# Kernel optimization log

Hardware: AMD Instinct MI355X
Metric: run time of the kernel (lower is better)

## Reference

```python
import jax, jax.numpy as jnp
import numpy as np

N = 50000      # nodes
E = 800000     # edges (avg degree 16)
IN = 128       # in_channels
C = 64         # hidden_channels (per-head out channels)
H = 8          # heads


def _lin(key, fan_in, fan_out):
    kw, kb = jax.random.split(key)
    scale = 1.0 / np.sqrt(fan_in)
    W = jax.random.uniform(kw, (fan_in, fan_out), jnp.float32, -scale, scale)
    b = jax.random.uniform(kb, (fan_out,), jnp.float32, -scale, scale)
    return W, b


def setup_inputs() -> dict:
    key = jax.random.key(0)
    ks = jax.random.split(key, 16)
    inp = {
        'x': jax.random.normal(ks[0], (N, IN), jnp.float32),
        'edge_index': jax.random.randint(ks[1], (2, E), 0, N, jnp.int64),
    }
    # layer 0: IN -> H*C (concat), layer 1: H*C -> H*C (concat), layer 2: H*C -> C (heads=1)
    dims = [(IN, H * C, H * C), (H * C, H * C, H * C), (H * C, C, C)]
    k = 2
    for i, (fi, fqkv, fskip) in enumerate(dims):
        for nm, fo in (('Wq', fqkv), ('Wk', fqkv), ('Wv', fqkv), ('Ws', fskip)):
            W, b = _lin(ks[k], fi, fo)
            inp[f'{nm}{i}'] = W
            inp[f'b{nm[1]}{i}'] = b
            k += 1
    return inp


def _conv(x, src, dst, Wq, bq, Wk, bk, Wv, bv, Ws, bs, heads, ch, concat):
    n = x.shape[0]
    q = (x @ Wq + bq).reshape(n, heads, ch)   # [N,H,C]
    k = (x @ Wk + bk).reshape(n, heads, ch)
    v = (x @ Wv + bv).reshape(n, heads, ch)
    # per-edge attention logits: [E,H]
    alpha = jnp.einsum('ehc,ehc->eh', q[dst], k[src]) / (ch ** 0.5)
    # segment softmax over incoming edges of each target node
    m = jax.ops.segment_max(alpha, dst, num_segments=n)
    m = jnp.where(jnp.isfinite(m), m, 0.0)
    ea = jnp.exp(alpha - m[dst])
    denom = jax.ops.segment_sum(ea, dst, num_segments=n) + 1e-16
    attn = ea / denom[dst]                    # [E,H]
    out = jax.ops.segment_sum(attn[:, :, None] * v[src], dst, num_segments=n)  # [N,H,C]
    out = out.reshape(n, heads * ch) if concat else out.mean(axis=1)
    # root/skip connection (beta=False)
    return out + x @ Ws + bs


def reference(x, edge_index,
              Wq0, bq0, Wk0, bk0, Wv0, bv0, Ws0, bs0,
              Wq1, bq1, Wk1, bk1, Wv1, bv1, Ws1, bs1,
              Wq2, bq2, Wk2, bk2, Wv2, bv2, Ws2, bs2):
    src, dst = edge_index[0], edge_index[1]
    h = _conv(x, src, dst, Wq0, bq0, Wk0, bk0, Wv0, bv0, Ws0, bs0, H, C, True)
    h = jax.nn.relu(h)
    h = _conv(h, src, dst, Wq1, bq1, Wk1, bk1, Wv1, bv1, Ws1, bs1, H, C, True)
    h = jax.nn.relu(h)
    out = _conv(h, src, dst, Wq2, bq2, Wk2, bk2, Wv2, bv2, Ws2, bs2, 1, C, False)
    return out
```

## Files before the change

### kernel.cpp

```cpp
#include <hip/hip_runtime.h>
#include <hip/hip_fp16.h>
#include <math.h>
#include <stdio.h>


using f16x8 = __attribute__((ext_vector_type(8))) _Float16;
using f32x4 = __attribute__((ext_vector_type(4))) float;

__device__ __forceinline__ void load_lds16(const void* g, void* l) {
  __builtin_amdgcn_global_load_lds((const __attribute__((address_space(1))) void*)g,
                                   (__attribute__((address_space(3))) void*)l,
                                   16, 0, 0);
}

__device__ __forceinline__ void fp8x4_to_f32(unsigned int w, float* o4) {
#if __has_builtin(__builtin_amdgcn_cvt_pk_f32_fp8)
  auto lo = __builtin_amdgcn_cvt_pk_f32_fp8(w, false);
  auto hi = __builtin_amdgcn_cvt_pk_f32_fp8(w, true);
  o4[0] = lo[0]; o4[1] = lo[1]; o4[2] = hi[0]; o4[3] = hi[1];
#else
#pragma unroll
  for (int t = 0; t < 4; ++t) {
    unsigned int b = (w >> (8 * t)) & 0xFFu;
    unsigned short h = (unsigned short)(((b & 0x80u) << 8) | ((b & 0x7Fu) << 7));
    __half hv = *(__half*)&h;
    o4[t] = (float)hv * 256.0f;
  }
#endif
}

__device__ __forceinline__ unsigned int fp8_pack2_sw(float a, float b) {
  unsigned int r = 0;
#pragma unroll
  for (int t = 0; t < 2; ++t) {
    float f = t ? b : a;
    __half h = __float2half(f * (1.0f / 256.0f));
    unsigned short hb = *(unsigned short*)&h;
    unsigned int sign = (hb >> 8) & 0x80u;
    unsigned int mag = (hb & 0x7FFFu) + 0x40u;
    unsigned int e = (mag >> 7) & 0x7Fu;
    if ((mag >> 7) > 0x7Eu) e = 0x7Eu;
    r |= (sign | e) << (8 * t);
  }
  return r;
}

__device__ __forceinline__ uint2 fp8_pack8(const float* f) {
#if __has_builtin(__builtin_amdgcn_cvt_pk_fp8_f32)
  int w0 = __builtin_amdgcn_cvt_pk_fp8_f32(f[0], f[1], 0, false);
  w0 = __builtin_amdgcn_cvt_pk_fp8_f32(f[2], f[3], w0, true);
  int w1 = __builtin_amdgcn_cvt_pk_fp8_f32(f[4], f[5], 0, false);
  w1 = __builtin_amdgcn_cvt_pk_fp8_f32(f[6], f[7], w1, true);
  uint2 r; r.x = (unsigned)w0; r.y = (unsigned)w1; return r;
#else
  uint2 r;
  r.x = fp8_pack2_sw(f[0], f[1]) | (fp8_pack2_sw(f[2], f[3]) << 16);
  r.y = fp8_pack2_sw(f[4], f[5]) | (fp8_pack2_sw(f[6], f[7]) << 16);
  return r;
#endif
}

__global__ void zero_misc_kernel(int* __restrict__ deg, __half* __restrict__ H,
                                 int N, int Npad) {
  int t = blockIdx.x * 256 + threadIdx.x;
  if (t < N) deg[t] = 0;
  int nz = (Npad - N) * 512 / 8;
  if (t < nz) {
    f16x8 z = {};
    *(f16x8*)(H + (size_t)N * 512 + (size_t)t * 8) = z;
  }
}

__global__ void degree_kernel(const int* __restrict__ dst, int* __restrict__ deg, int E) {
  int e = blockIdx.x * blockDim.x + threadIdx.x;
  if (e < E) atomicAdd(&deg[dst[e]], 1);
}

__global__ __launch_bounds__(256)
void scan_a_kernel(const int* __restrict__ deg, int* __restrict__ rowptr,
                   int* __restrict__ bsum, int n) {
  __shared__ int tmp[256];
  int t = threadIdx.x;
  int i = blockIdx.x * 256 + t;
  int v = (i < n) ? deg[i] : 0;
  tmp[t] = v;
  __syncthreads();
#pragma unroll
  for (int off = 1; off < 256; off <<= 1) {
    int u = (t >= off) ? tmp[t - off] : 0;
    __syncthreads();
    tmp[t] += u;
    __syncthreads();
  }
  if (i < n) rowptr[i + 1] = tmp[t];
  if (t == 255) bsum[blockIdx.x] = tmp[255];
}

__global__ __launch_bounds__(256)
void scan_b_kernel(int* __restrict__ bsum, int nb) {
  __shared__ int tmp[256];
  int t = threadIdx.x;
  int v = (t < nb) ? bsum[t] : 0;
  tmp[t] = v;
  __syncthreads();
#pragma unroll
  for (int off = 1; off < 256; off <<= 1) {
    int u = (t >= off) ? tmp[t - off] : 0;
    __syncthreads();
    tmp[t] += u;
    __syncthreads();
  }
  if (t < nb) bsum[t] = tmp[t] - v;
}

__global__ __launch_bounds__(256)
void scan_c_kernel(int* __restrict__ rowptr, int* __restrict__ cursor,
                   const int* __restrict__ bsum, int n) {
  int i = blockIdx.x * 256 + threadIdx.x;
  if (i < n) {
    int r = rowptr[i + 1] + bsum[blockIdx.x];
    rowptr[i + 1] = r;
    cursor[i + 1] = r;
  }
  if (i == 0) { rowptr[0] = 0; cursor[0] = 0; }
}

__global__ void scatter_kernel(const int* __restrict__ src, const int* __restrict__ dst,
                               int* __restrict__ cursor, int* __restrict__ col, int E) {
  int e = blockIdx.x * blockDim.x + threadIdx.x;
  if (e < E) {
    int pos = atomicAdd(&cursor[dst[e]], 1);
    col[pos] = src[e];
  }
}

__global__ __launch_bounds__(256)
void transpose_all_kernel(
    const float* __restrict__ Wq0, const float* __restrict__ Wk0,
    const float* __restrict__ Wv0, const float* __restrict__ Ws0,
    const float* __restrict__ Wq1, const float* __restrict__ Wk1,
    const float* __restrict__ Wv1, const float* __restrict__ Ws1,
    const float* __restrict__ Wq2, const float* __restrict__ Wk2,
    const float* __restrict__ Wv2, const float* __restrict__ Ws2,
    __half* __restrict__ Wt) {
  int z = blockIdx.z;
  int layer = z >> 2, m = z & 3;
  int K = (layer == 0) ? 128 : 512;
  int D = (layer == 2) ? 64 : 512;
  int c0 = blockIdx.x * 32, k0 = blockIdx.y * 32;
  if (c0 >= D || k0 >= K) return;
  const float* W;
  switch (z) {
    case 0: W = Wq0; break; case 1: W = Wk0; break;
    case 2: W = Wv0; break; case 3: W = Ws0; break;
    case 4: W = Wq1; break; case 5: W = Wk1; break;
    case 6: W = Wv1; break; case 7: W = Ws1; break;
    case 8: W = Wq2; break; case 9: W = Wk2; break;
    case 10: W = Wv2; break; default: W = Ws2; break;
  }
  __half* dstBase = Wt + ((layer == 0) ? 0 : (layer == 1) ? 262144 : 1310720);
  __shared__ float t[32][33];
  int tx = threadIdx.x & 31, ty = threadIdx.x >> 5;
#pragma unroll
  for (int r = 0; r < 4; ++r)
    t[ty + 8 * r][tx] = W[(size_t)(k0 + ty + 8 * r) * D + c0 + tx];
  __syncthreads();
#pragma unroll
  for (int r = 0; r < 4; ++r)
    dstBase[(size_t)(m * D + c0 + ty + 8 * r) * K + k0 + tx] =
        __float2half(t[tx][ty + 8 * r]);
}

__global__ void bias_all_kernel(
    const float* __restrict__ b0, const float* __restrict__ b1,
    const float* __restrict__ b2, const float* __restrict__ b3,
    const float* __restrict__ b4, const float* __restrict__ b5,
    const float* __restrict__ b6, const float* __restrict__ b7,
    const float* __restrict__ b8, const float* __restrict__ b9,
    const float* __restrict__ b10, const float* __restrict__ b11,
    float* __restrict__ bias_arena) {
  int z = blockIdx.x;
  int layer = z >> 2, m = z & 3;
  int D = (layer == 2) ? 64 : 512;
  const float* b;
  switch (z) {
    case 0: b = b0; break; case 1: b = b1; break;
    case 2: b = b2; break; case 3: b = b3; break;
    case 4: b = b4; break; case 5: b = b5; break;
    case 6: b = b6; break; case 7: b = b7; break;
    case 8: b = b8; break; case 9: b = b9; break;
    case 10: b = b10; break; default: b = b11; break;
  }
  float* dst = bias_arena + ((layer == 0) ? 0 : (layer == 1) ? 2048 : 4096) + m * D;
  for (int c = threadIdx.x; c < D; c += 256) dst[c] = b[c];
}

template <int LAYER>
__global__ __launch_bounds__(256, 2)
void gemm_mfma_kernel(const void* __restrict__ Avoid,
                      const __half* __restrict__ Wt,
                      const float* __restrict__ bias,
                      __half* __restrict__ QS, __half* __restrict__ KV,
                      int Nrows) {
  constexpr int K = (LAYER == 0) ? 128 : 512;
  constexpr int lda = (LAYER == 0) ? 128 : 512;
  constexpr int NT = (LAYER == 2) ? 1 : 8;
  constexpr int NSTEP = K / 32;
  __shared__ __align__(16) char smem_raw[49152];
  __half* sm = (__half*)smem_raw;
  int tid = threadIdx.x;
  int wave = tid >> 6, lane = tid & 63;
  int wr = wave >> 1, wc = wave & 1;
  int bid = blockIdx.x;
  int xcd = bid & 7;
  int r = bid >> 3;
  int n0 = (r % NT) * 256;
  int m0 = ((r / NT) * 8 + xcd) * 128;
  int srow = lane >> 2;
  int sslot = lane & 3;
  int skc = (sslot ^ ((srow >> 1) & 3)) << 3;
  int quad = lane >> 4, rr = lane & 15;
  int rslot = (quad ^ ((rr >> 1) & 3)) << 3;

  f32x4 acc[4][8] = {};

  auto stage = [&](int buf, int kt) {
    __half* As = sm + buf * 12288;
    __half* Bs = As + 4096;
#pragma unroll
    for (int p = 0; p < 2; ++p) {
      int rbase = wave * 32 + p * 16;
      if constexpr (LAYER == 0) {
        int row = m0 + rbase + srow;
        const float* ga = (const float*)Avoid + (size_t)row * lda + kt + skc;
        f16x8 hv = {};
        if (row < Nrows) {
          float4 f0 = *(const float4*)ga;
          float4 f1 = *(const float4*)(ga + 4);
          hv[0] = (_Float16)f0.x; hv[1] = (_Float16)f0.y;
          hv[2] = (_Float16)f0.z; hv[3] = (_Float16)f0.w;
          hv[4] = (_Float16)f1.x; hv[5] = (_Float16)f1.y;
          hv[6] = (_Float16)f1.z; hv[7] = (_Float16)f1.w;
        }
        *(f16x8*)&As[(rbase + srow) * 32 + sslot * 8] = hv;
      } else {
        const __half* ga = (const __half*)Avoid +
                           (size_t)(m0 + rbase + srow) * lda + kt + skc;
        load_lds16(ga, &As[rbase * 32]);
      }
    }
#pragma unroll
    for (int p = 0; p < 4; ++p) {
      int rbase = wave * 64 + p * 16;
      const __half* gb = Wt + (size_t)(n0 + rbase + srow) * K + kt + skc;
      load_lds16(gb, &Bs[rbase * 32]);
    }
  };

  stage(0, 0);
  __syncthreads();

  for (int t = 0; t < NSTEP; ++t) {
    if (t + 1 < NSTEP) stage((t + 1) & 1, (t + 1) * 32);
    const __half* As = sm + (t & 1) * 12288;
    const __half* Bs = As + 4096;
    f16x8 a[4], b[8];
#pragma unroll
    for (int i = 0; i < 4; ++i) {
      int row = wr * 64 + i * 16 + rr;
      a[i] = *(const f16x8*)&As[row * 32 + rslot];
    }
#pragma unroll
    for (int j = 0; j < 8; ++j) {
      int row = wc * 128 + j * 16 + rr;
      b[j] = *(const f16x8*)&Bs[row * 32 + rslot];
    }
#pragma unroll
    for (int i = 0; i < 4; ++i)
#pragma unroll
      for (int j = 0; j < 8; ++j)
        acc[i][j] = __builtin_amdgcn_mfma_f32_16x16x32_f16(a[i], b[j], acc[i][j], 0, 0, 0);
    __syncthreads();
  }

  int cl = lane & 15, rb = (lane >> 4) * 4;

  if constexpr (LAYER == 2) {
    __half* S = (__half*)smem_raw;
#pragma unroll
    for (int round = 0; round < 2; ++round) {
      if (wr == round) {
#pragma unroll
        for (int i = 0; i < 4; ++i)
#pragma unroll
          for (int j = 0; j < 8; ++j) {
            int colL = wc * 128 + j * 16 + cl;
            float bj = bias[colL];
#pragma unroll
            for (int rg = 0; rg < 4; ++rg) {
              int rowL = i * 16 + rb + rg;
              S[rowL * 264 + colL] = __float2half(acc[i][j][rg] + bj);
            }
          }
      }
      __syncthreads();
#pragma unroll
      for (int it = 0; it < 8; ++it) {
        int id = it * 256 + tid;
        int rowL = id >> 5, ch = id & 31;
        int grow = m0 + round * 64 + rowL;
        int colb = ch * 8;
        int seg = colb >> 6, c = colb & 63;
        __half* base = (seg == 0) ? QS + (size_t)grow * 128 + c
                     : (seg == 3) ? QS + (size_t)grow * 128 + 64 + c
                     : (seg == 1) ? KV + (size_t)grow * 128 + c
                                  : KV + (size_t)grow * 128 + 64 + c;
        *(f16x8*)base = *(const f16x8*)&S[rowL * 264 + colb];
      }
      __syncthreads();
    }
  } else {
    const int msegB = n0 >> 9;
    const int cb = n0 & 511;
    if (msegB == 0 || msegB == 3) {
      __half* S = (__half*)smem_raw;
      const int coff = (msegB == 3) ? 512 : 0;
#pragma unroll
      for (int round = 0; round < 2; ++round) {
        if (wr == round) {
#pragma unroll
          for (int i = 0; i < 4; ++i)
#pragma unroll
            for (int j = 0; j < 8; ++j) {
              int colL = wc * 128 + j * 16 + cl;
              float bj = bias[n0 + colL];
#pragma unroll
              for (int rg = 0; rg < 4; ++rg) {
                int rowL = i * 16 + rb + rg;
                S[rowL * 264 + colL] = __float2half(acc[i][j][rg] + bj);
              }
            }
        }
        __syncthreads();
#pragma unroll
        for (int it = 0; it < 8; ++it) {
          int id = it * 256 + tid;
          int rowL = id >> 5, ch = id & 31;
          int grow = m0 + round * 64 + rowL;
          int colb = ch * 8;
          *(f16x8*)(QS + (size_t)grow * 1024 + coff + cb + colb) =
              *(const f16x8*)&S[rowL * 264 + colb];
        }
        __syncthreads();
      }
    } else {
      float* S = (float*)smem_raw;
      unsigned char* KV8 = (unsigned char*)KV;
      const int koff = (msegB == 2) ? 8 : 0;
#pragma unroll
      for (int round = 0; round < 4; ++round) {
        if (wr == (round >> 1)) {
#pragma unroll
          for (int ii = 0; ii < 2; ++ii) {
#pragma unroll
            for (int j = 0; j < 8; ++j) {
              int colL = wc * 128 + j * 16 + cl;
              float bj = bias[n0 + colL];
#pragma unroll
              for (int rg = 0; rg < 4; ++rg) {
                int rowL = ii * 16 + rb + rg;
                S[rowL * 260 + colL] = acc[(round & 1) * 2 + ii][j][rg] + bj;
              }
            }
          }
        }
        __syncthreads();
#pragma unroll
        for (int it = 0; it < 4; ++it) {
          int id = it * 256 + tid;
          int rowL = id >> 5, ch = id & 31;
          int grow = m0 + round * 32 + rowL;
          int colb = ch * 8;
          float f[8];
          f32x4 lo = *(const f32x4*)&S[rowL * 260 + colb];
          f32x4 hi = *(const f32x4*)&S[rowL * 260 + colb + 4];
          f[0] = lo[0]; f[1] = lo[1]; f[2] = lo[2]; f[3] = lo[3];
          f[4] = hi[0]; f[5] = hi[1]; f[6] = hi[2]; f[7] = hi[3];
          uint2 pk = fp8_pack8(f);
          *(uint2*)(KV8 + (size_t)grow * 1024 + ((cb + colb) >> 3) * 16 + koff) = pk;
        }
        __syncthreads();
      }
    }
  }
}

__global__ __launch_bounds__(256)
void attn_h8_kernel(const __half* __restrict__ QS, const unsigned char* __restrict__ KV8,
                    const int* __restrict__ rowptr, const int* __restrict__ col,
                    __half* __restrict__ Hout, int N) {
  int n = blockIdx.x * 4 + (threadIdx.x >> 6);
  if (n >= N) return;
  int lane = threadIdx.x & 63;
  size_t rbase = (size_t)n * 1024 + lane * 8;

  f16x8 qv = __builtin_nontemporal_load((const f16x8*)(QS + rbase));
  float qf[8];
#pragma unroll
  for (int j = 0; j < 8; ++j) qf[j] = (float)qv[j];

  int e0 = rowptr[n], e1 = rowptr[n + 1];
  float m = -INFINITY, l = 0.f;
  float o[8] = {};

  const uint4* KVL = (const uint4*)KV8;
  uint4 ea = {}, eb = {};
  int i = e0;
  if (i < e1)     ea = KVL[(size_t)col[i] * 64 + lane];
  if (i + 1 < e1) eb = KVL[(size_t)col[i + 1] * 64 + lane];

  while (i < e1) {
    int rem = e1 - i;
    uint4 ec = {}, ed = {};
    if (rem > 2) ec = KVL[(size_t)col[i + 2] * 64 + lane];
    if (rem > 3) ed = KVL[(size_t)col[i + 3] * 64 + lane];
    float ka[8], kb[8];
    fp8x4_to_f32(ea.x, ka); fp8x4_to_f32(ea.y, ka + 4);
    fp8x4_to_f32(eb.x, kb); fp8x4_to_f32(eb.y, kb + 4);
    float pa = 0.f, pb = 0.f;
#pragma unroll
    for (int j = 0; j < 8; ++j) { pa += ka[j] * qf[j]; pb += kb[j] * qf[j]; }
    pa += __shfl_xor(pa, 1, 64); pb += __shfl_xor(pb, 1, 64);
    pa += __shfl_xor(pa, 2, 64); pb += __shfl_xor(pb, 2, 64);
    pa += __shfl_xor(pa, 4, 64); pb += __shfl_xor(pb, 4, 64);
    float a0 = pa * 0.125f;
    float va[8];
    fp8x4_to_f32(ea.z, va); fp8x4_to_f32(ea.w, va + 4);
    if (rem > 1) {
      float vb[8];
      fp8x4_to_f32(eb.z, vb); fp8x4_to_f32(eb.w, vb + 4);
      float a1 = pb * 0.125f;
      float mn = fmaxf(m, fmaxf(a0, a1));
      float sc = __expf(m - mn);
      float ex0 = __expf(a0 - mn), ex1 = __expf(a1 - mn);
      l = l * sc + ex0 + ex1;
#pragma unroll
      for (int c = 0; c < 8; ++c)
        o[c] = o[c] * sc + ex0 * va[c] + ex1 * vb[c];
      m = mn;
    } else {
      float mn = fmaxf(m, a0);
      float sc = __expf(m - mn);
      float ex0 = __expf(a0 - mn);
      l = l * sc + ex0;
#pragma unroll
      for (int c = 0; c < 8; ++c) o[c] = o[c] * sc + ex0 * va[c];
      m = mn;
    }
    ea = ec; eb = ed;
    i += 2;
  }

  float inv = 1.f / (l + 1e-16f);
  f16x8 sv = __builtin_nontemporal_load((const f16x8*)(QS + rbase + 512));
  f16x8 hv;
#pragma unroll
  for (int c = 0; c < 8; ++c) {
    float r = o[c] * inv + (float)sv[c];
    hv[c] = (_Float16)fmaxf(r, 0.f);
  }
  __builtin_nontemporal_store(hv, (f16x8*)(Hout + (size_t)n * 512 + lane * 8));
}

__global__ __launch_bounds__(256)
void attn_h1_kernel(const __half* __restrict__ QS, const __half* __restrict__ KV,
                    const int* __restrict__ rowptr, const int* __restrict__ col,
                    float* __restrict__ out, int N) {
  int n = (blockIdx.x * 256 + threadIdx.x) >> 3;
  if (n >= N) return;
  int gl = threadIdx.x & 7;
  size_t rbase = (size_t)n * 128 + gl * 8;

  f16x8 qv = __builtin_nontemporal_load((const f16x8*)(QS + rbase));
  float qf[8];
#pragma unroll
  for (int j = 0; j < 8; ++j) qf[j] = (float)qv[j];

  int e0 = rowptr[n], e1 = rowptr[n + 1];
  float m = -INFINITY, l = 0.f;
  float o[8] = {};

  f16x8 ka = {}, va = {}, kb = {}, vb = {};
  int i = e0;
  if (i < e1) {
    const __half* p = KV + (size_t)col[i] * 128 + gl * 8;
    ka = *(const f16x8*)p; va = *(const f16x8*)(p + 64);
  }
  if (i + 1 < e1) {
    const __half* p = KV + (size_t)col[i + 1] * 128 + gl * 8;
    kb = *(const f16x8*)p; vb = *(const f16x8*)(p + 64);
  }

  while (i < e1) {
    int rem = e1 - i;
    f16x8 kc = {}, vc = {}, kd = {}, vd = {};
    if (rem > 2) {
      const __half* p = KV + (size_t)col[i + 2] * 128 + gl * 8;
      kc = *(const f16x8*)p; vc = *(const f16x8*)(p + 64);
    }
    if (rem > 3) {
      const __half* p = KV + (size_t)col[i + 3] * 128 + gl * 8;
      kd = *(const f16x8*)p; vd = *(const f16x8*)(p + 64);
    }
    float pa = 0.f, pb = 0.f;
#pragma unroll
    for (int j = 0; j < 8; ++j) { pa += (float)ka[j] * qf[j]; pb += (float)kb[j] * qf[j]; }
    pa += __shfl_xor(pa, 1, 64); pb += __shfl_xor(pb, 1, 64);
    pa += __shfl_xor(pa, 2, 64); pb += __shfl_xor(pb, 2, 64);
    pa += __shfl_xor(pa, 4, 64); pb += __shfl_xor(pb, 4, 64);
    float a0 = pa * 0.125f;
    if (rem > 1) {
      float a1 = pb * 0.125f;
      float mn = fmaxf(m, fmaxf(a0, a1));
      float sc = __expf(m - mn);
      float ea = __expf(a0 - mn), eb = __expf(a1 - mn);
      l = l * sc + ea + eb;
#pragma unroll
      for (int c = 0; c < 8; ++c)
        o[c] = o[c] * sc + ea * (float)va[c] + eb * (float)vb[c];
      m = mn;
    } else {
      float mn = fmaxf(m, a0);
      float sc = __expf(m - mn);
      float ea = __expf(a0 - mn);
      l = l * sc + ea;
#pragma unroll
      for (int c = 0; c < 8; ++c) o[c] = o[c] * sc + ea * (float)va[c];
      m = mn;
    }
    ka = kc; va = vc; kb = kd; vb = vd;
    i += 2;
  }

  float inv = 1.f / (l + 1e-16f);
  f16x8 sv = __builtin_nontemporal_load((const f16x8*)(QS + rbase + 64));
  f32x4 r0, r1;
#pragma unroll
  for (int c = 0; c < 4; ++c) r0[c] = o[c] * inv + (float)sv[c];
#pragma unroll
  for (int c = 0; c < 4; ++c) r1[c] = o[c + 4] * inv + (float)sv[c + 4];
  float* op = out + (size_t)n * 64 + gl * 8;
  *(f32x4*)op = r0;
  *(f32x4*)(op + 4) = r1;
}

extern "C" void kernel_launch(void* const* d_in, const int* in_sizes, int n_in,
                              void* d_out, int out_size, void* d_ws, size_t ws_size,
                              hipStream_t stream) {
  const float* x = (const float*)d_in[0];
  const int* ei = (const int*)d_in[1];
  const int N = in_sizes[0] / 128;
  const int E = in_sizes[1] / 2;
  const int Npad = ((N + 1023) / 1024) * 1024;
  const int mtiles = Npad / 128;
  const int* srcp = ei;
  const int* dstp = ei + E;

  const float* Wq0 = (const float*)d_in[2];  const float* bq0 = (const float*)d_in[3];
  const float* Wk0 = (const float*)d_in[4];  const float* bk0 = (const float*)d_in[5];
  const float* Wv0 = (const float*)d_in[6];  const float* bv0 = (const float*)d_in[7];
  const float* Ws0 = (const float*)d_in[8];  const float* bs0 = (const float*)d_in[9];
  const float* Wq1 = (const float*)d_in[10]; const float* bq1 = (const float*)d_in[11];
  const float* Wk1 = (const float*)d_in[12]; const float* bk1 = (const float*)d_in[13];
  const float* Wv1 = (const float*)d_in[14]; const float* bv1 = (const float*)d_in[15];
  const float* Ws1 = (const float*)d_in[16]; const float* bs1 = (const float*)d_in[17];
  const float* Wq2 = (const float*)d_in[18]; const float* bq2 = (const float*)d_in[19];
  const float* Wk2 = (const float*)d_in[20]; const float* bk2 = (const float*)d_in[21];
  const float* Wv2 = (const float*)d_in[22]; const float* bv2 = (const float*)d_in[23];
  const float* Ws2 = (const float*)d_in[24]; const float* bs2 = (const float*)d_in[25];

  char* p = (char*)d_ws;
  __half* QS = (__half*)p;               p += (size_t)Npad * 1024 * 2;
  __half* KV = (__half*)p;               p += (size_t)Npad * 1024;
  __half* H  = (__half*)p;               p += (size_t)Npad * 512 * 2;
  __half* Wt = (__half*)p;               p += (size_t)1441792 * 2;
  float* bias_arena = (float*)p;         p += 4352 * 4;
  int* deg    = (int*)p;                 p += (size_t)N * 4;
  int* rowptr = (int*)p;                 p += (size_t)(N + 1) * 4;
  int* cursor = (int*)p;                 p += (size_t)(N + 1) * 4;
  int* colv   = (int*)p;                 p += (size_t)E * 4;
  int* bsum   = (int*)p;                 p += 256 * 4;
  size_t need = p - (char*)d_ws;
  if (ws_size < need) {
    fprintf(stderr, "kernel_launch: ws_size=%zu < need=%zu — aborting cleanly\n",
            ws_size, need);
    return;
  }

  const int nscan = (N + 255) / 256;

  transpose_all_kernel<<<dim3(16, 16, 12), 256, 0, stream>>>(
      Wq0, Wk0, Wv0, Ws0, Wq1, Wk1, Wv1, Ws1, Wq2, Wk2, Wv2, Ws2, Wt);
  bias_all_kernel<<<12, 256, 0, stream>>>(
      bq0, bk0, bv0, bs0, bq1, bk1, bv1, bs1, bq2, bk2, bv2, bs2, bias_arena);
  zero_misc_kernel<<<((Npad - N) * 512 / 8 + 255) / 256 > (N + 255) / 256
                         ? ((Npad - N) * 512 / 8 + 255) / 256
                         : (N + 255) / 256,
                    256, 0, stream>>>(deg, H, N, Npad);

  degree_kernel<<<(E + 255) / 256, 256, 0, stream>>>(dstp, deg, E);
  scan_a_kernel<<<nscan, 256, 0, stream>>>(deg, rowptr, bsum, N);
  scan_b_kernel<<<1, 256, 0, stream>>>(bsum, nscan);
  scan_c_kernel<<<nscan, 256, 0, stream>>>(rowptr, cursor, bsum, N);
  scatter_kernel<<<(E + 255) / 256, 256, 0, stream>>>(srcp, dstp, cursor, colv, E);

  __half* Wt0 = Wt;
  __half* Wt1 = Wt + 262144;
  __half* Wt2 = Wt + 1310720;

  gemm_mfma_kernel<0><<<mtiles * 8, 256, 0, stream>>>(
      x, Wt0, bias_arena, QS, KV, N);
  attn_h8_kernel<<<(N + 3) / 4, 256, 0, stream>>>(QS, (const unsigned char*)KV,
                                                  rowptr, colv, H, N);

  gemm_mfma_kernel<1><<<mtiles * 8, 256, 0, stream>>>(
      H, Wt1, bias_arena + 2048, QS, KV, Npad);
  attn_h8_kernel<<<(N + 3) / 4, 256, 0, stream>>>(QS, (const unsigned char*)KV,
                                                  rowptr, colv, H, N);

  gemm_mfma_kernel<2><<<mtiles, 256, 0, stream>>>(
      H, Wt2, bias_arena + 4096, QS, KV, Npad);
  attn_h1_kernel<<<(N + 31) / 32, 256, 0, stream>>>(QS, KV, rowptr, colv,
                                                    (float*)d_out, N);
}
```

Measured before the change: 747.1 us.

## Triple-buffer GEMM k-loop with async LDS loads and pre-convert x to fp16

The GEMM main loop moves from a double-buffered stage with full __syncthreads to a three-stage pipeline. It uses explicit vmcnt waits, split barriers and raised wave priority during the MFMA block, so global-to-LDS loads overlap more compute. Layer 0's input is converted to fp16 by a separate kernel, which lets all layers use the direct global_load_lds path. In exchange the LDS footprint grows to 72KB per block, which may cut occupancy below the launch bound of 2, and the extra conversion pass adds a launch and traffic.

```diff
diff --git a/kernel.cpp b/kernel.cpp
--- a/kernel.cpp
+++ b/kernel.cpp
@@ -69,6 +69,24 @@
     f16x8 z = {};
     *(f16x8*)(H + (size_t)N * 512 + (size_t)t * 8) = z;
   }
+}
+
+__global__ void convert_x_kernel(const float* __restrict__ x, __half* __restrict__ xh,
+                                 int N, int Npad) {
+  int t = blockIdx.x * 256 + threadIdx.x;
+  if (t >= Npad * 16) return;
+  int row = t >> 4;
+  f16x8 hv = {};
+  if (row < N) {
+    const float* g = x + (size_t)t * 8;
+    float4 f0 = *(const float4*)g;
+    float4 f1 = *(const float4*)(g + 4);
+    hv[0] = (_Float16)f0.x; hv[1] = (_Float16)f0.y;
+    hv[2] = (_Float16)f0.z; hv[3] = (_Float16)f0.w;
+    hv[4] = (_Float16)f1.x; hv[5] = (_Float16)f1.y;
+    hv[6] = (_Float16)f1.z; hv[7] = (_Float16)f1.w;
+  }
+  *(f16x8*)(xh + (size_t)t * 8) = hv;
 }
 
 __global__ void degree_kernel(const int* __restrict__ dst, int* __restrict__ deg, int E) {
@@ -197,16 +215,15 @@
 
 template <int LAYER>
 __global__ __launch_bounds__(256, 2)
-void gemm_mfma_kernel(const void* __restrict__ Avoid,
+void gemm_mfma_kernel(const __half* __restrict__ Aptr,
                       const __half* __restrict__ Wt,
                       const float* __restrict__ bias,
-                      __half* __restrict__ QS, __half* __restrict__ KV,
-                      int Nrows) {
+                      __half* __restrict__ QS, __half* __restrict__ KV) {
   constexpr int K = (LAYER == 0) ? 128 : 512;
   constexpr int lda = (LAYER == 0) ? 128 : 512;
   constexpr int NT = (LAYER == 2) ? 1 : 8;
   constexpr int NSTEP = K / 32;
-  __shared__ __align__(16) char smem_raw[49152];
+  __shared__ __align__(16) char smem_raw[73728];
   __half* sm = (__half*)smem_raw;
   int tid = threadIdx.x;
   int wave = tid >> 6, lane = tid & 63;
@@ -230,24 +247,8 @@
 #pragma unroll
     for (int p = 0; p < 2; ++p) {
       int rbase = wave * 32 + p * 16;
-      if constexpr (LAYER == 0) {
-        int row = m0 + rbase + srow;
-        const float* ga = (const float*)Avoid + (size_t)row * lda + kt + skc;
-        f16x8 hv = {};
-        if (row < Nrows) {
-          float4 f0 = *(const float4*)ga;
-          float4 f1 = *(const float4*)(ga + 4);
-          hv[0] = (_Float16)f0.x; hv[1] = (_Float16)f0.y;
-          hv[2] = (_Float16)f0.z; hv[3] = (_Float16)f0.w;
-          hv[4] = (_Float16)f1.x; hv[5] = (_Float16)f1.y;
-          hv[6] = (_Float16)f1.z; hv[7] = (_Float16)f1.w;
-        }
-        *(f16x8*)&As[(rbase + srow) * 32 + sslot * 8] = hv;
-      } else {
-        const __half* ga = (const __half*)Avoid +
-                           (size_t)(m0 + rbase + srow) * lda + kt + skc;
-        load_lds16(ga, &As[rbase * 32]);
-      }
+      const __half* ga = Aptr + (size_t)(m0 + rbase + srow) * lda + kt + skc;
+      load_lds16(ga, &As[rbase * 32]);
     }
 #pragma unroll
     for (int p = 0; p < 4; ++p) {
@@ -258,11 +259,16 @@
   };
 
   stage(0, 0);
-  __syncthreads();
+  stage(1, 32);
+  stage(2, 64);
 
   for (int t = 0; t < NSTEP; ++t) {
-    if (t + 1 < NSTEP) stage((t + 1) & 1, (t + 1) * 32);
-    const __half* As = sm + (t & 1) * 12288;
+    if (t + 2 < NSTEP)      asm volatile("s_waitcnt vmcnt(12)" ::: "memory");
+    else if (t + 1 < NSTEP) asm volatile("s_waitcnt vmcnt(6)" ::: "memory");
+    else                    asm volatile("s_waitcnt vmcnt(0)" ::: "memory");
+    __builtin_amdgcn_s_barrier();
+
+    const __half* As = sm + (t % 3) * 12288;
     const __half* Bs = As + 4096;
     f16x8 a[4], b[8];
 #pragma unroll
@@ -275,13 +281,21 @@
       int row = wc * 128 + j * 16 + rr;
       b[j] = *(const f16x8*)&Bs[row * 32 + rslot];
     }
+    asm volatile("s_waitcnt lgkmcnt(0)" ::: "memory");
+    __builtin_amdgcn_sched_barrier(0);
+    __builtin_amdgcn_s_barrier();
+
+    if (t + 3 < NSTEP) stage(t % 3, (t + 3) * 32);
+
+    __builtin_amdgcn_s_setprio(1);
 #pragma unroll
     for (int i = 0; i < 4; ++i)
 #pragma unroll
       for (int j = 0; j < 8; ++j)
         acc[i][j] = __builtin_amdgcn_mfma_f32_16x16x32_f16(a[i], b[j], acc[i][j], 0, 0, 0);
-    __syncthreads();
-  }
+    __builtin_amdgcn_s_setprio(0);
+  }
+  __syncthreads();
 
   int cl = lane & 15, rb = (lane >> 4) * 4;
 
@@ -583,6 +597,7 @@
   __half* QS = (__half*)p;               p += (size_t)Npad * 1024 * 2;
   __half* KV = (__half*)p;               p += (size_t)Npad * 1024;
   __half* H  = (__half*)p;               p += (size_t)Npad * 512 * 2;
+  __half* xh = (__half*)p;               p += (size_t)Npad * 128 * 2;
   __half* Wt = (__half*)p;               p += (size_t)1441792 * 2;
   float* bias_arena = (float*)p;         p += 4352 * 4;
   int* deg    = (int*)p;                 p += (size_t)N * 4;
@@ -607,6 +622,7 @@
                          ? ((Npad - N) * 512 / 8 + 255) / 256
                          : (N + 255) / 256,
                     256, 0, stream>>>(deg, H, N, Npad);
+  convert_x_kernel<<<(Npad * 16 + 255) / 256, 256, 0, stream>>>(x, xh, N, Npad);
 
   degree_kernel<<<(E + 255) / 256, 256, 0, stream>>>(dstp, deg, E);
   scan_a_kernel<<<nscan, 256, 0, stream>>>(deg, rowptr, bsum, N);
@@ -619,17 +635,17 @@
   __half* Wt2 = Wt + 1310720;
 
   gemm_mfma_kernel<0><<<mtiles * 8, 256, 0, stream>>>(
-      x, Wt0, bias_arena, QS, KV, N);
+      xh, Wt0, bias_arena, QS, KV);
   attn_h8_kernel<<<(N + 3) / 4, 256, 0, stream>>>(QS, (const unsigned char*)KV,
                                                   rowptr, colv, H, N);
 
   gemm_mfma_kernel<1><<<mtiles * 8, 256, 0, stream>>>(
-      H, Wt1, bias_arena + 2048, QS, KV, Npad);
+      H, Wt1, bias_arena + 2048, QS, KV);
   attn_h8_kernel<<<(N + 3) / 4, 256, 0, stream>>>(QS, (const unsigned char*)KV,
                                                   rowptr, colv, H, N);
 
   gemm_mfma_kernel<2><<<mtiles, 256, 0, stream>>>(
-      H, Wt2, bias_arena + 4096, QS, KV, Npad);
+      H, Wt2, bias_arena + 4096, QS, KV);
   attn_h1_kernel<<<(N + 31) / 32, 256, 0, stream>>>(QS, KV, rowptr, colv,
                                                     (float*)d_out, N);
 }
```

Measured after the change: 719.2 us. 3.7% less time.
